# Performance work log

Measured on AMD Instinct MI355X. Metric: run time of the kernel, lower is better.

Reference implementation:

```python
import jax, jax.numpy as jnp
import numpy as np

MAGNITUDE = 9
PROB = 0.5
WARP_STRENGTH = MAGNITUDE * 0.3 / 9.0  # = 0.3


def _notaknot_matrix(S):
    # System for second derivatives M of a cubic spline on uniform grid h=1
    # (scipy CubicSpline default bc_type='not-a-knot').
    A = np.zeros((S, S), dtype=np.float32)
    i = np.arange(1, S - 1)
    A[i, i - 1] = 1.0
    A[i, i] = 4.0
    A[i, i + 1] = 1.0
    # not-a-knot: third derivative continuous at x1 and x_{S-2}
    A[0, 0], A[0, 1], A[0, 2] = 1.0, -2.0, 1.0
    A[-1, -3], A[-1, -2], A[-1, -1] = 1.0, -2.0, 1.0
    return A


def setup_inputs() -> dict:
    key = jax.random.key(0)
    k1, k2, k3 = jax.random.split(key, 3)
    B, C, S = 128, 64, 4096
    x = jax.random.normal(k1, (B, C, S), dtype=jnp.float32)
    # per-sample scale ~ U(1 - warp_strength, 1 + warp_strength)
    scale = (1.0 - WARP_STRENGTH) + 2.0 * WARP_STRENGTH * jax.random.uniform(k2, (B,), dtype=jnp.float32)
    # per-sample apply decision: rand < prob
    apply_mask = jax.random.uniform(k3, (B,)) < PROB
    return {"x": x, "scale": scale, "apply_mask": apply_mask}


def reference(x, scale, apply_mask):
    B, C, S = x.shape
    A = jnp.asarray(_notaknot_matrix(S))  # (S, S), fixed uniform-grid system

    # --- fit not-a-knot cubic splines for all B*C signals at once ---
    y = x.reshape(B * C, S)
    rhs = jnp.zeros_like(y).at[:, 1:-1].set(
        6.0 * (y[:, :-2] - 2.0 * y[:, 1:-1] + y[:, 2:])
    )  # not-a-knot rows have rhs 0
    M = jnp.linalg.solve(A, rhs.T).T.reshape(B, C, S)  # second derivatives

    # --- warped evaluation points (shared across channels of a sample) ---
    grid = jnp.arange(S, dtype=x.dtype)
    w = jnp.clip(grid[None, :] * scale[:, None], 0.0, S - 1)  # (B, S)
    idx = jnp.clip(jnp.floor(w).astype(jnp.int32), 0, S - 2)  # interval index
    t = (w - idx.astype(x.dtype))[:, None, :]                 # (B, 1, S)

    idx3 = jnp.broadcast_to(idx[:, None, :], (B, C, S))
    y0 = jnp.take_along_axis(x, idx3, axis=2)
    y1 = jnp.take_along_axis(x, idx3 + 1, axis=2)
    M0 = jnp.take_along_axis(M, idx3, axis=2)
    M1 = jnp.take_along_axis(M, idx3 + 1, axis=2)

    # s(t) = y0 + b t + c t^2 + d t^3 on each unit interval (h = 1)
    b = (y1 - y0) - (2.0 * M0 + M1) / 6.0
    c = M0 / 2.0
    d = (M1 - M0) / 6.0
    warped = y0 + t * (b + t * (c + t * d))

    return jnp.where(apply_mask[:, None, None], warped, x)
```

## Files before the change

kernel.cpp:

```cpp
#include <hip/hip_runtime.h>
#include <math.h>


#define SLEN 4096
#define WRAD 8
#define BLK  256
#define NG   4

__global__ __launch_bounds__(BLK, 3) void time_warp_kernel(
    const float* __restrict__ x,
    const float* __restrict__ scale,
    const int*   __restrict__ apply_mask,
    float* __restrict__ out,
    int C)
{
    __shared__ float sy[SLEN];
    __shared__ float sf[SLEN + 2 * WRAD];
    __shared__ float sm[SLEN];

    const int bid = blockIdx.x;
    const int b   = bid / C;
    const int t   = threadIdx.x;
    const float* __restrict__ xin = x   + (size_t)bid * SLEN;
    float*       __restrict__ o   = out + (size_t)bid * SLEN;

    if (apply_mask[b] == 0) {
        const float4* __restrict__ xi4 = (const float4*)xin;
        float4*       __restrict__ o4  = (float4*)o;
        #pragma unroll
        for (int s = 0; s < NG; ++s)
            o4[t + BLK * s] = xi4[t + BLK * s];
        return;
    }

    {
        const float4* __restrict__ xi4 = (const float4*)xin;
        #pragma unroll
        for (int s = 0; s < NG; ++s)
            *(float4*)&sy[4 * t + 1024 * s] = xi4[t + BLK * s];
    }
    if (t < WRAD)                      sf[t] = 0.0f;
    else if (t >= 16 && t < 16 + WRAD) sf[(SLEN + 2 * WRAD - 1) - (t - 16)] = 0.0f;
    __syncthreads();

    const float M1  = sy[0]        - 2.0f * sy[1]        + sy[2];
    const float MS2 = sy[SLEN - 3] - 2.0f * sy[SLEN - 2] + sy[SLEN - 1];

    #pragma unroll
    for (int s = 0; s < NG; ++s) {
        const int j0 = 4 * t + 1024 * s;
        float4 yc = *(const float4*)&sy[j0];
        float  ym = (j0 > 0)        ? sy[j0 - 1] : 0.0f;
        float  yp = (j0 + 4 < SLEN) ? sy[j0 + 4] : 0.0f;
        float yv[6] = {ym, yc.x, yc.y, yc.z, yc.w, yp};
        float fe[4];
        #pragma unroll
        for (int e = 0; e < 4; ++e) {
            const int j = j0 + e;
            float v = 6.0f * (yv[e] - 2.0f * yv[e + 1] + yv[e + 2]);
            if (j < 2 || j > SLEN - 3) v = 0.0f;
            if (j == 2)        v -= M1;
            if (j == SLEN - 3) v -= MS2;
            fe[e] = v;
        }
        *(float4*)&sf[WRAD + j0] = make_float4(fe[0], fe[1], fe[2], fe[3]);
    }
    __syncthreads();

    const float r = 0.26794919243112270f;
    float G[WRAD + 1];
    G[0] = 0.28867513459481287f;
    #pragma unroll
    for (int k = 1; k <= WRAD; ++k) G[k] = -G[k - 1] * r;
    const float log2r = -1.8999686269529532f;

    float v1 = 0.0f, vS2 = 0.0f;
    #pragma unroll
    for (int k = 1; k <= WRAD; ++k) {
        v1  += G[k] * sf[WRAD + 1 + k];
        vS2 += G[k] * sf[WRAD + (SLEN - 2) - k];
    }

    #pragma unroll
    for (int s = 0; s < NG; ++s) {
        const int j0 = 4 * t + 1024 * s;
        float fw[4 * (WRAD / 4) * 2 + 4];
        #pragma unroll
        for (int m = 0; m < 5; ++m)
            *(float4*)&fw[4 * m] = *(const float4*)&sf[j0 + 4 * m];
        float mv[4];
        #pragma unroll
        for (int e = 0; e < 4; ++e) {
            float acc = G[0] * fw[WRAD + e];
            #pragma unroll
            for (int k = 1; k <= WRAD; ++k)
                acc += G[k] * (fw[WRAD + e - k] + fw[WRAD + e + k]);
            const int i = j0 + e;
            if (i >= 2 && i <= 34) {
                float cc = v1 * exp2f((float)(i - 1) * log2r);
                acc += (i & 1) ? -cc : cc;
            }
            if (i >= SLEN - 36 && i <= SLEN - 3) {
                float cc = vS2 * exp2f((float)(SLEN - 2 - i) * log2r);
                acc += (i & 1) ? cc : -cc;
            }
            mv[e] = acc;
        }
        if (j0 == 0)        { mv[1] = M1;  mv[0] = 2.0f * M1  - mv[2]; }
        if (j0 == SLEN - 4) { mv[2] = MS2; mv[3] = 2.0f * MS2 - mv[1]; }
        *(float4*)&sm[j0] = make_float4(mv[0], mv[1], mv[2], mv[3]);
    }
    __syncthreads();

    const float sc = scale[b];
    #pragma unroll
    for (int s = 0; s < NG; ++s) {
        const int j0 = 4 * t + 1024 * s;
        float rv[4];
        #pragma unroll
        for (int e = 0; e < 4; ++e) {
            const int j = j0 + e;
            float w = fminf((float)j * sc, (float)(SLEN - 1));
            int idx = (int)w;
            if (idx > SLEN - 2) idx = SLEN - 2;
            float tt  = w - (float)idx;
            float y0  = sy[idx];
            float y1  = sy[idx + 1];
            float m0  = sm[idx];
            float m1v = sm[idx + 1];
            float bb = (y1 - y0) - (2.0f * m0 + m1v) * (1.0f / 6.0f);
            float cc = 0.5f * m0;
            float dd = (m1v - m0) * (1.0f / 6.0f);
            rv[e] = y0 + tt * (bb + tt * (cc + tt * dd));
        }
        ((float4*)o)[t + BLK * s] = make_float4(rv[0], rv[1], rv[2], rv[3]);
    }
}

extern "C" void kernel_launch(void* const* d_in, const int* in_sizes, int n_in,
                              void* d_out, int out_size, void* d_ws, size_t ws_size,
                              hipStream_t stream) {
    const float* x     = (const float*)d_in[0];
    const float* scale = (const float*)d_in[1];
    const int*   mask  = (const int*)d_in[2];
    float*       out   = (float*)d_out;

    const int B     = in_sizes[1];
    const int total = in_sizes[0];
    const int C     = total / (B * SLEN);
    const int nblk  = B * C;

    time_warp_kernel<<<nblk, BLK, 0, stream>>>(x, scale, mask, out, C);
}
```

Before: 233.4 us.

## Fold RHS stencil into spline filter taps and drop intermediate shared buffer

Precomposes the second-difference RHS stencil with the truncated inverse filter into a wider 19-tap kernel applied directly to the input samples in shared memory. This removes the separate RHS pass, its shared array and one barrier for interior chunks; only boundary chunks keep the old exact path. Shared memory drops from three arrays to two, so launch bounds rise to five blocks per CU for more occupancy. The gather stage now writes scalars in a strided pattern using nontemporal stores, and the copy path also uses nontemporal stores. The cost is more FLOPs per output and a slightly different rounding order.

```diff
diff --git a/kernel.cpp b/kernel.cpp
--- a/kernel.cpp
+++ b/kernel.cpp
@@ -5,9 +5,10 @@
 #define SLEN 4096
 #define WRAD 8
 #define BLK  256
-#define NG   4
 
-__global__ __launch_bounds__(BLK, 3) void time_warp_kernel(
+typedef float f32x4 __attribute__((ext_vector_type(4)));
+
+__global__ __launch_bounds__(BLK, 5) void time_warp_kernel(
     const float* __restrict__ x,
     const float* __restrict__ scale,
     const int*   __restrict__ apply_mask,
@@ -15,7 +16,6 @@
     int C)
 {
     __shared__ float sy[SLEN];
-    __shared__ float sf[SLEN + 2 * WRAD];
     __shared__ float sm[SLEN];
 
     const int bid = blockIdx.x;
@@ -25,45 +25,21 @@
     float*       __restrict__ o   = out + (size_t)bid * SLEN;
 
     if (apply_mask[b] == 0) {
-        const float4* __restrict__ xi4 = (const float4*)xin;
-        float4*       __restrict__ o4  = (float4*)o;
+        const f32x4* __restrict__ xi4 = (const f32x4*)xin;
+        f32x4*       __restrict__ o4  = (f32x4*)o;
         #pragma unroll
-        for (int s = 0; s < NG; ++s)
-            o4[t + BLK * s] = xi4[t + BLK * s];
+        for (int k = 0; k < 4; ++k) {
+            f32x4 v = xi4[t + BLK * k];
+            __builtin_nontemporal_store(v, &o4[t + BLK * k]);
+        }
         return;
     }
 
     {
         const float4* __restrict__ xi4 = (const float4*)xin;
         #pragma unroll
-        for (int s = 0; s < NG; ++s)
-            *(float4*)&sy[4 * t + 1024 * s] = xi4[t + BLK * s];
-    }
-    if (t < WRAD)                      sf[t] = 0.0f;
-    else if (t >= 16 && t < 16 + WRAD) sf[(SLEN + 2 * WRAD - 1) - (t - 16)] = 0.0f;
-    __syncthreads();
-
-    const float M1  = sy[0]        - 2.0f * sy[1]        + sy[2];
-    const float MS2 = sy[SLEN - 3] - 2.0f * sy[SLEN - 2] + sy[SLEN - 1];
-
-    #pragma unroll
-    for (int s = 0; s < NG; ++s) {
-        const int j0 = 4 * t + 1024 * s;
-        float4 yc = *(const float4*)&sy[j0];
-        float  ym = (j0 > 0)        ? sy[j0 - 1] : 0.0f;
-        float  yp = (j0 + 4 < SLEN) ? sy[j0 + 4] : 0.0f;
-        float yv[6] = {ym, yc.x, yc.y, yc.z, yc.w, yp};
-        float fe[4];
-        #pragma unroll
-        for (int e = 0; e < 4; ++e) {
-            const int j = j0 + e;
-            float v = 6.0f * (yv[e] - 2.0f * yv[e + 1] + yv[e + 2]);
-            if (j < 2 || j > SLEN - 3) v = 0.0f;
-            if (j == 2)        v -= M1;
-            if (j == SLEN - 3) v -= MS2;
-            fe[e] = v;
-        }
-        *(float4*)&sf[WRAD + j0] = make_float4(fe[0], fe[1], fe[2], fe[3]);
+        for (int k = 0; k < 4; ++k)
+            *(float4*)&sy[4 * (t + BLK * k)] = xi4[t + BLK * k];
     }
     __syncthreads();
 
@@ -72,68 +48,109 @@
     G[0] = 0.28867513459481287f;
     #pragma unroll
     for (int k = 1; k <= WRAD; ++k) G[k] = -G[k - 1] * r;
+    float Hh[WRAD + 2];
+    Hh[0] = 12.0f * (G[1] - G[0]);
+    #pragma unroll
+    for (int k = 1; k < WRAD; ++k) Hh[k] = 6.0f * (G[k - 1] - 2.0f * G[k] + G[k + 1]);
+    Hh[WRAD]     = 6.0f * (G[WRAD - 1] - 2.0f * G[WRAD]);
+    Hh[WRAD + 1] = 6.0f * G[WRAD];
     const float log2r = -1.8999686269529532f;
 
-    float v1 = 0.0f, vS2 = 0.0f;
     #pragma unroll
-    for (int k = 1; k <= WRAD; ++k) {
-        v1  += G[k] * sf[WRAD + 1 + k];
-        vS2 += G[k] * sf[WRAD + (SLEN - 2) - k];
-    }
+    for (int s = 0; s < 4; ++s) {
+        const int j0 = 4 * t + 1024 * s;
+        if (j0 >= 36 && j0 <= SLEN - 44) {
+            float wv[28];
+            #pragma unroll
+            for (int m = 0; m < 7; ++m)
+                *(float4*)&wv[4 * m] = *(const float4*)&sy[j0 - 12 + 4 * m];
+            float mv[4];
+            #pragma unroll
+            for (int e = 0; e < 4; ++e) {
+                float acc = Hh[0] * wv[12 + e];
+                #pragma unroll
+                for (int k = 1; k <= WRAD + 1; ++k)
+                    acc += Hh[k] * (wv[12 + e - k] + wv[12 + e + k]);
+                mv[e] = acc;
+            }
+            *(float4*)&sm[j0] = make_float4(mv[0], mv[1], mv[2], mv[3]);
+        } else {
+            const float M1  = sy[0]        - 2.0f * sy[1]        + sy[2];
+            const float MS2 = sy[SLEN - 3] - 2.0f * sy[SLEN - 2] + sy[SLEN - 1];
 
-    #pragma unroll
-    for (int s = 0; s < NG; ++s) {
-        const int j0 = 4 * t + 1024 * s;
-        float fw[4 * (WRAD / 4) * 2 + 4];
-        #pragma unroll
-        for (int m = 0; m < 5; ++m)
-            *(float4*)&fw[4 * m] = *(const float4*)&sf[j0 + 4 * m];
-        float mv[4];
-        #pragma unroll
-        for (int e = 0; e < 4; ++e) {
-            float acc = G[0] * fw[WRAD + e];
+            float v1 = 0.0f, vS2 = 0.0f;
             #pragma unroll
-            for (int k = 1; k <= WRAD; ++k)
-                acc += G[k] * (fw[WRAD + e - k] + fw[WRAD + e + k]);
-            const int i = j0 + e;
-            if (i >= 2 && i <= 34) {
-                float cc = v1 * exp2f((float)(i - 1) * log2r);
-                acc += (i & 1) ? -cc : cc;
+            for (int k = 1; k <= WRAD; ++k) {
+                const int ja = 1 + k;
+                float fa = 6.0f * (sy[ja - 1] - 2.0f * sy[ja] + sy[ja + 1]);
+                if (ja == 2) fa -= M1;
+                v1 += G[k] * fa;
+                const int jb = SLEN - 2 - k;
+                float fb = 6.0f * (sy[jb - 1] - 2.0f * sy[jb] + sy[jb + 1]);
+                if (jb == SLEN - 3) fb -= MS2;
+                vS2 += G[k] * fb;
             }
-            if (i >= SLEN - 36 && i <= SLEN - 3) {
-                float cc = vS2 * exp2f((float)(SLEN - 2 - i) * log2r);
-                acc += (i & 1) ? cc : -cc;
+
+            float wv[28];
+            #pragma unroll
+            for (int m = 0; m < 7; ++m) {
+                const int q = j0 - 12 + 4 * m;
+                float4 v = make_float4(0.0f, 0.0f, 0.0f, 0.0f);
+                if (q >= 0 && q <= SLEN - 4) v = *(const float4*)&sy[q];
+                *(float4*)&wv[4 * m] = v;
             }
-            mv[e] = acc;
+            float fw[20];
+            #pragma unroll
+            for (int p = 0; p < 20; ++p) {
+                const int jj = j0 + p - 8;
+                float fv = 6.0f * (wv[p + 3] - 2.0f * wv[p + 4] + wv[p + 5]);
+                if (jj < 2 || jj > SLEN - 3) fv = 0.0f;
+                if (jj == 2)        fv -= M1;
+                if (jj == SLEN - 3) fv -= MS2;
+                fw[p] = fv;
+            }
+            float mv[4];
+            #pragma unroll
+            for (int e = 0; e < 4; ++e) {
+                float acc = G[0] * fw[8 + e];
+                #pragma unroll
+                for (int k = 1; k <= WRAD; ++k)
+                    acc += G[k] * (fw[8 + e - k] + fw[8 + e + k]);
+                const int i = j0 + e;
+                if (i >= 2 && i <= 34) {
+                    float cc = v1 * exp2f((float)(i - 1) * log2r);
+                    acc += (i & 1) ? -cc : cc;
+                }
+                if (i >= SLEN - 36 && i <= SLEN - 3) {
+                    float cc = vS2 * exp2f((float)(SLEN - 2 - i) * log2r);
+                    acc += (i & 1) ? cc : -cc;
+                }
+                mv[e] = acc;
+            }
+            if (j0 == 0)        { mv[1] = M1;  mv[0] = 2.0f * M1  - mv[2]; }
+            if (j0 == SLEN - 4) { mv[2] = MS2; mv[3] = 2.0f * MS2 - mv[1]; }
+            *(float4*)&sm[j0] = make_float4(mv[0], mv[1], mv[2], mv[3]);
         }
-        if (j0 == 0)        { mv[1] = M1;  mv[0] = 2.0f * M1  - mv[2]; }
-        if (j0 == SLEN - 4) { mv[2] = MS2; mv[3] = 2.0f * MS2 - mv[1]; }
-        *(float4*)&sm[j0] = make_float4(mv[0], mv[1], mv[2], mv[3]);
     }
     __syncthreads();
 
     const float sc = scale[b];
     #pragma unroll
-    for (int s = 0; s < NG; ++s) {
-        const int j0 = 4 * t + 1024 * s;
-        float rv[4];
-        #pragma unroll
-        for (int e = 0; e < 4; ++e) {
-            const int j = j0 + e;
-            float w = fminf((float)j * sc, (float)(SLEN - 1));
-            int idx = (int)w;
-            if (idx > SLEN - 2) idx = SLEN - 2;
-            float tt  = w - (float)idx;
-            float y0  = sy[idx];
-            float y1  = sy[idx + 1];
-            float m0  = sm[idx];
-            float m1v = sm[idx + 1];
-            float bb = (y1 - y0) - (2.0f * m0 + m1v) * (1.0f / 6.0f);
-            float cc = 0.5f * m0;
-            float dd = (m1v - m0) * (1.0f / 6.0f);
-            rv[e] = y0 + tt * (bb + tt * (cc + tt * dd));
-        }
-        ((float4*)o)[t + BLK * s] = make_float4(rv[0], rv[1], rv[2], rv[3]);
+    for (int q = 0; q < 16; ++q) {
+        const int j = t + BLK * q;
+        float w = fminf((float)j * sc, (float)(SLEN - 1));
+        int idx = (int)w;
+        if (idx > SLEN - 2) idx = SLEN - 2;
+        const float tt  = w - (float)idx;
+        const float y0  = sy[idx];
+        const float y1  = sy[idx + 1];
+        const float m0  = sm[idx];
+        const float m1v = sm[idx + 1];
+        const float bb = (y1 - y0) - (2.0f * m0 + m1v) * (1.0f / 6.0f);
+        const float cc = 0.5f * m0;
+        const float dd = (m1v - m0) * (1.0f / 6.0f);
+        const float res = y0 + tt * (bb + tt * (cc + tt * dd));
+        __builtin_nontemporal_store(res, &o[j]);
     }
 }
 
```

Result: no change. 237.9 us (+1.9%).
